# Kernel optimization log

Hardware: AMD Instinct MI355X
Metric: run time of the kernel (lower is better)

## Reference

```python
import jax, jax.numpy as jnp
import numpy as np

# Render constants matching GaussianRenderer(__init__): image size and top-K blend depth.
H, W, K = 128, 128, 10
N_G = 2048  # number of gaussians


def setup_inputs() -> dict:
    key = jax.random.key(0)
    k1, k2, k3, k4 = jax.random.split(key, 4)
    # Means in pixel coordinates so gaussians cover the image.
    gaussian_means = jax.random.uniform(k1, (N_G, 2), dtype=jnp.float32) * jnp.array([W, H], jnp.float32)
    # Rotation angle per gaussian in [0, 2pi).
    gaussian_rotations = jax.random.uniform(k2, (N_G,), dtype=jnp.float32) * (2.0 * np.pi)
    # log std-devs centered at log(3) => ~3px footprint.
    gaussian_log_scales = jax.random.normal(k3, (N_G, 2), dtype=jnp.float32) * 0.3 + np.log(3.0)
    gaussian_colors = jax.random.uniform(k4, (N_G, 3), dtype=jnp.float32)
    return {
        "gaussian_means": gaussian_means,
        "gaussian_rotations": gaussian_rotations,
        "gaussian_log_scales": gaussian_log_scales,
        "gaussian_colors": gaussian_colors,
    }


def reference(gaussian_means, gaussian_rotations, gaussian_log_scales, gaussian_colors):
    """2D Gaussian splatting: per-pixel top-K gaussians by opacity, alpha-composited.

    Covariance per gaussian: Sigma = R(theta) diag(exp(2*log_scales)) R(theta)^T.
    alpha_i(p) = exp(-0.5 * d^T Sigma^{-1} d), d = p - mean_i.
    Per pixel, the K gaussians with largest alpha are blended front-to-back:
        out = sum_i color_i * alpha_i * prod_{j<i} (1 - alpha_j).
    (The torch module's tile binning + max_G_per_tile is a GPU performance
    optimization; the dense evaluation here computes the same per-pixel math.)
    """
    cos_t = jnp.cos(gaussian_rotations)  # [N]
    sin_t = jnp.sin(gaussian_rotations)
    inv_var = jnp.exp(-2.0 * gaussian_log_scales)  # [N,2] = 1/sigma^2 per axis
    ivx, ivy = inv_var[:, 0], inv_var[:, 1]
    # Sigma^{-1} = R diag(1/sx^2, 1/sy^2) R^T  (symmetric 2x2: [[a, b], [b, c]])
    a = cos_t * cos_t * ivx + sin_t * sin_t * ivy  # [N]
    c = sin_t * sin_t * ivx + cos_t * cos_t * ivy
    b = cos_t * sin_t * (ivx - ivy)

    xs = jnp.arange(W, dtype=jnp.float32) + 0.5
    ys = jnp.arange(H, dtype=jnp.float32) + 0.5
    px, py = jnp.meshgrid(xs, ys)  # [H,W] each
    dx = px.reshape(-1, 1) - gaussian_means[:, 0]  # [P, N], P = H*W
    dy = py.reshape(-1, 1) - gaussian_means[:, 1]
    q = a * dx * dx + 2.0 * b * dx * dy + c * dy * dy  # Mahalanobis distance^2 [P,N]
    alpha = jnp.exp(-0.5 * q)  # [P,N] in (0,1]

    top_alpha, top_idx = jax.lax.top_k(alpha, K)  # [P,K], descending alpha
    # Front-to-back transmittance: T_0 = 1, T_i = prod_{j<i} (1 - alpha_j)
    trans = jnp.cumprod(1.0 - top_alpha, axis=1)
    trans = jnp.concatenate([jnp.ones_like(trans[:, :1]), trans[:, :-1]], axis=1)
    weight = top_alpha * trans  # [P,K]
    top_colors = gaussian_colors[top_idx]  # [P,K,3]
    image = jnp.einsum("pk,pkc->pc", weight, top_colors).reshape(H, W, 3)
    return image
```

## Files before the change

kernel.cpp:

```cpp
#include <hip/hip_runtime.h>

#define HH 128
#define WW 128
#define NPX (HH * WW)
#define KK 10
#define PXB 16
#define LCAP 352
#define JMAX 22
#define KEYC 6
#define SCAP (16 * KEYC)
#define SPAD (SCAP + 1)
#define ALPHA_MIN 5e-4f
#define RADIUS_K 3.8990f

typedef unsigned long long u64;
typedef unsigned int u32;

__global__ __launch_bounds__(256) void precompute_kernel(
    const float* __restrict__ means, const float* __restrict__ rots,
    const float* __restrict__ lscales, int nG,
    float4* __restrict__ bbox4, float4* __restrict__ prm4) {
  int g = blockIdx.x * blockDim.x + threadIdx.x;
  if (g >= nG) return;
  const float2* m2 = (const float2*)means;
  const float2* l2 = (const float2*)lscales;
  float2 mg = m2[g];
  float2 lg = l2[g];
  float smx = __expf(fmaxf(lg.x, lg.y));
  float r = fmaf(RADIUS_K * 1.01f, smx, 0.05f);
  float th = rots[g];
  float s = __sinf(th), c = __cosf(th);
  float ivx = __expf(-2.0f * lg.x);
  float ivy = __expf(-2.0f * lg.y);
  bbox4[g] = make_float4(mg.x, mg.y, r * r, 0.0f);
  prm4[g] = make_float4(c * c * ivx + s * s * ivy,
                        2.0f * (c * s * (ivx - ivy)),
                        s * s * ivx + c * c * ivy, mg.x);
}

template <int NGC, bool PRE>
__global__ __launch_bounds__(256) void splat_kernel(
    const float* __restrict__ means, const float* __restrict__ rots,
    const float* __restrict__ lscales, const float* __restrict__ cols,
    const float4* __restrict__ bbox4, const float4* __restrict__ prm4,
    int nG_rt, float* __restrict__ out) {
  const int nG = NGC > 0 ? NGC : nG_rt;
  __shared__ float4 sA[LCAP];
  __shared__ float  sMy[LCAP];
  __shared__ int    glist[LCAP];
  __shared__ float2 sbuf[PXB][SPAD];
  __shared__ float2 wbuf[PXB][KK];
  __shared__ int    lcnt;

  int t = threadIdx.x;
  int lane = t & 63;
  int pl  = t >> 4;
  int tsl = t & 15;
  int tile = blockIdx.x;
  int x0 = (tile & 31) << 2, y0 = (tile >> 5) << 2;
  int x = x0 | (pl & 3), y = y0 | (pl >> 2);
  float px = (float)x + 0.5f, py = (float)y + 0.5f;

  if (t == 0) lcnt = 0;
  __syncthreads();

  float rx0 = (float)x0 + 0.5f, rx1 = (float)x0 + 3.5f;
  float ry0 = (float)y0 + 0.5f, ry1 = (float)y0 + 3.5f;
  if (PRE && NGC > 0) {
    constexpr int FR = ((NGC > 0 ? NGC : 1) + 255) / 256;
    float4 bb[FR];
#pragma unroll
    for (int j = 0; j < FR; ++j) {
      int g = t + (j << 8);
      bb[j] = (g < NGC) ? bbox4[g] : make_float4(-1e30f, -1e30f, 0.0f, 0.0f);
    }
#pragma unroll
    for (int j = 0; j < FR; ++j) {
      float4 b = bb[j];
      float cx = fminf(fmaxf(b.x, rx0), rx1) - b.x;
      float cy = fminf(fmaxf(b.y, ry0), ry1) - b.y;
      bool hit = (cx * cx + cy * cy <= b.z);
      u64 mask = __ballot(hit);
      if (mask) {
        int leader = __ffsll((unsigned long long)mask) - 1;
        int base;
        if (lane == leader) base = atomicAdd(&lcnt, __popcll(mask));
        base = __shfl(base, leader);
        if (hit) {
          int idx = base + __popcll(mask & ((1ull << lane) - 1ull));
          if (idx < LCAP) {
            int g = t + (j << 8);
            sA[idx] = prm4[g];
            sMy[idx] = b.y;
            glist[idx] = g;
          }
        }
      }
    }
  } else if (PRE) {
    for (int g = t; g < nG; g += 256) {
      float4 b = bbox4[g];
      float cx = fminf(fmaxf(b.x, rx0), rx1) - b.x;
      float cy = fminf(fmaxf(b.y, ry0), ry1) - b.y;
      bool hit = (cx * cx + cy * cy <= b.z);
      u64 mask = __ballot(hit);
      if (mask) {
        int leader = __ffsll((unsigned long long)mask) - 1;
        int base;
        if (lane == leader) base = atomicAdd(&lcnt, __popcll(mask));
        base = __shfl(base, leader);
        if (hit) {
          int idx = base + __popcll(mask & ((1ull << lane) - 1ull));
          if (idx < LCAP) {
            sA[idx] = prm4[g];
            sMy[idx] = b.y;
            glist[idx] = g;
          }
        }
      }
    }
  } else {
    const float2* m2 = (const float2*)means;
    const float2* l2 = (const float2*)lscales;
    for (int g = t; g < nG; g += 256) {
      float2 mg = m2[g];
      float2 lg = l2[g];
      float smx = __expf(fmaxf(lg.x, lg.y));
      float r = fmaf(RADIUS_K * 1.01f, smx, 0.05f);
      float cx = fminf(fmaxf(mg.x, rx0), rx1) - mg.x;
      float cy = fminf(fmaxf(mg.y, ry0), ry1) - mg.y;
      bool hit = (cx * cx + cy * cy <= r * r);
      u64 mask = __ballot(hit);
      if (mask) {
        int leader = __ffsll((unsigned long long)mask) - 1;
        int base;
        if (lane == leader) base = atomicAdd(&lcnt, __popcll(mask));
        base = __shfl(base, leader);
        if (hit) {
          int idx = base + __popcll(mask & ((1ull << lane) - 1ull));
          if (idx < LCAP) {
            float th = rots[g];
            float s = __sinf(th), c = __cosf(th);
            float ivx = __expf(-2.0f * lg.x);
            float ivy = __expf(-2.0f * lg.y);
            sA[idx] = make_float4(c * c * ivx + s * s * ivy,
                                  2.0f * (c * s * (ivx - ivy)),
                                  s * s * ivx + c * c * ivy, mg.x);
            sMy[idx] = mg.y;
            glist[idx] = g;
          }
        }
      }
    }
  }
  __syncthreads();
  int cnt = min(lcnt, LCAP);
  int jcnt = (cnt + 15) >> 4;

  float ra[JMAX];
  float mymax = 0.0f;
#pragma unroll
  for (int j = 0; j < JMAX; ++j) {
    float a = 0.0f;
    if (j < jcnt) {
      int i = tsl + (j << 4);
      if (i < cnt) {
        float4 q0 = sA[i];
        float dx = px - q0.w, dy = py - sMy[i];
        float q = fmaf(dx, fmaf(q0.y, dy, q0.x * dx), q0.z * dy * dy);
        a = __expf(-0.5f * q);
      }
    }
    ra[j] = a;
    mymax = fmaxf(mymax, a);
  }

  float v = mymax;
#pragma unroll
  for (int k = 2; k <= 16; k <<= 1) {
#pragma unroll
    for (int j = k >> 1; j >= 1; j >>= 1) {
      float o = __shfl_xor(v, j, 16);
      bool keepMax = (((tsl & k) == 0) == ((tsl & j) == 0));
      v = keepMax ? fmaxf(v, o) : fminf(v, o);
    }
  }
  float tau = fmaxf(__shfl(v, 9, 16), ALPHA_MIN);

  int cpx = 0;
  int grp = lane >> 4;
#pragma unroll
  for (int j = 0; j < JMAX; ++j) {
    if (j < jcnt) {
      bool s = ra[j] >= tau;
      u64 mask = __ballot(s);
      u32 sub = (u32)((mask >> (grp * 16)) & 0xFFFFull);
      if (s) {
        int idx = cpx + __popc(sub & ((1u << tsl) - 1u));
        if (idx < SCAP)
          sbuf[pl][idx] = make_float2(ra[j], __int_as_float(glist[tsl + (j << 4)]));
      }
      cpx += __popc(sub);
    }
  }
  int scp = min(cpx, SCAP);
  int nw = min(scp, KK);

#pragma unroll
  for (int c = 0; c < KEYC; ++c) {
    if ((c << 4) < scp) {
      int i = tsl + (c << 4);
      u64 kc = 0;
      if (i < scp) {
        float2 e = sbuf[pl][i];
        kc = ((u64)__float_as_uint(e.x) << 32) | (u32)(~(u32)__float_as_int(e.y));
      }
      int rk = 0;
      for (int s2 = 0; s2 < scp; ++s2) {
        float2 e2 = sbuf[pl][s2];
        u64 ks2 = ((u64)__float_as_uint(e2.x) << 32) |
                  (u32)(~(u32)__float_as_int(e2.y));
        rk += (kc < ks2) ? 1 : 0;
      }
      if (kc != 0 && rk < KK)
        wbuf[pl][rk] = make_float2(__uint_as_float((u32)(kc >> 32)),
                                   __int_as_float((int)(~(u32)kc)));
    }
  }

  float my_alpha = 0.0f;
  int my_id = 0;
  if (tsl < nw) {
    float2 e = wbuf[pl][tsl];
    my_alpha = e.x;
    my_id = __float_as_int(e.y);
  }

  float T = 1.0f - my_alpha;
#pragma unroll
  for (int d = 1; d < 16; d <<= 1) {
    float u = __shfl_up(T, d, 16);
    if (tsl >= d) T *= u;
  }
  float ex = __shfl_up(T, 1, 16);
  if (tsl == 0) ex = 1.0f;
  float w = my_alpha * ex;
  float cr = 0.0f, cg = 0.0f, cb = 0.0f;
  if (my_alpha > 0.0f) {
    cr = w * cols[3 * my_id + 0];
    cg = w * cols[3 * my_id + 1];
    cb = w * cols[3 * my_id + 2];
  }
#pragma unroll
  for (int d = 1; d < 16; d <<= 1) {
    cr += __shfl_xor(cr, d);
    cg += __shfl_xor(cg, d);
    cb += __shfl_xor(cb, d);
  }
  int p = y * WW + x;
  if (tsl < 3) out[3 * p + tsl] = (tsl == 0) ? cr : ((tsl == 1) ? cg : cb);
}

extern "C" void kernel_launch(void* const* d_in, const int* in_sizes, int n_in,
                              void* d_out, int out_size, void* d_ws, size_t ws_size,
                              hipStream_t stream) {
  const float* means   = (const float*)d_in[0];
  const float* rots    = (const float*)d_in[1];
  const float* lscales = (const float*)d_in[2];
  const float* cols    = (const float*)d_in[3];
  float* out = (float*)d_out;
  int nG = in_sizes[1];

  size_t need = (size_t)nG * sizeof(float4) * 2;
  bool pre = (d_ws != nullptr) && (ws_size >= need);
  float4* bbox4 = (float4*)d_ws;
  float4* prm4 = (float4*)((char*)d_ws + (size_t)nG * sizeof(float4));

  if (pre)
    precompute_kernel<<<(nG + 255) / 256, 256, 0, stream>>>(means, rots,
                                                            lscales, nG,
                                                            bbox4, prm4);

  if (nG == 2048) {
    if (pre)
      splat_kernel<2048, true><<<NPX / PXB, 256, 0, stream>>>(
          means, rots, lscales, cols, bbox4, prm4, nG, out);
    else
      splat_kernel<2048, false><<<NPX / PXB, 256, 0, stream>>>(
          means, rots, lscales, cols, nullptr, nullptr, nG, out);
  } else {
    if (pre)
      splat_kernel<0, true><<<NPX / PXB, 256, 0, stream>>>(
          means, rots, lscales, cols, bbox4, prm4, nG, out);
    else
      splat_kernel<0, false><<<NPX / PXB, 256, 0, stream>>>(
          means, rots, lscales, cols, nullptr, nullptr, nG, out);
  }
}
```

Measured before the change: 69.75 us.

## Drop precompute kernel; compute conic params in-block after culling

Measured after the change: 68.22 us. 1.02x faster.

```diff
diff --git a/kernel.cpp b/kernel.cpp
--- a/kernel.cpp
+++ b/kernel.cpp
@@ -16,33 +16,10 @@
 typedef unsigned long long u64;
 typedef unsigned int u32;
 
-__global__ __launch_bounds__(256) void precompute_kernel(
-    const float* __restrict__ means, const float* __restrict__ rots,
-    const float* __restrict__ lscales, int nG,
-    float4* __restrict__ bbox4, float4* __restrict__ prm4) {
-  int g = blockIdx.x * blockDim.x + threadIdx.x;
-  if (g >= nG) return;
-  const float2* m2 = (const float2*)means;
-  const float2* l2 = (const float2*)lscales;
-  float2 mg = m2[g];
-  float2 lg = l2[g];
-  float smx = __expf(fmaxf(lg.x, lg.y));
-  float r = fmaf(RADIUS_K * 1.01f, smx, 0.05f);
-  float th = rots[g];
-  float s = __sinf(th), c = __cosf(th);
-  float ivx = __expf(-2.0f * lg.x);
-  float ivy = __expf(-2.0f * lg.y);
-  bbox4[g] = make_float4(mg.x, mg.y, r * r, 0.0f);
-  prm4[g] = make_float4(c * c * ivx + s * s * ivy,
-                        2.0f * (c * s * (ivx - ivy)),
-                        s * s * ivx + c * c * ivy, mg.x);
-}
-
-template <int NGC, bool PRE>
+template <int NGC>
 __global__ __launch_bounds__(256) void splat_kernel(
     const float* __restrict__ means, const float* __restrict__ rots,
     const float* __restrict__ lscales, const float* __restrict__ cols,
-    const float4* __restrict__ bbox4, const float4* __restrict__ prm4,
     int nG_rt, float* __restrict__ out) {
   const int nG = NGC > 0 ? NGC : nG_rt;
   __shared__ float4 sA[LCAP];
@@ -64,71 +41,26 @@
   if (t == 0) lcnt = 0;
   __syncthreads();
 
+  const float2* m2 = (const float2*)means;
+  const float2* l2 = (const float2*)lscales;
   float rx0 = (float)x0 + 0.5f, rx1 = (float)x0 + 3.5f;
   float ry0 = (float)y0 + 0.5f, ry1 = (float)y0 + 3.5f;
-  if (PRE && NGC > 0) {
+  if (NGC > 0) {
     constexpr int FR = ((NGC > 0 ? NGC : 1) + 255) / 256;
-    float4 bb[FR];
+    float2 mg[FR], lg[FR];
 #pragma unroll
     for (int j = 0; j < FR; ++j) {
       int g = t + (j << 8);
-      bb[j] = (g < NGC) ? bbox4[g] : make_float4(-1e30f, -1e30f, 0.0f, 0.0f);
+      bool v = g < NGC;
+      mg[j] = v ? m2[g] : make_float2(-1e30f, -1e30f);
+      lg[j] = v ? l2[g] : make_float2(0.0f, 0.0f);
     }
 #pragma unroll
     for (int j = 0; j < FR; ++j) {
-      float4 b = bb[j];
-      float cx = fminf(fmaxf(b.x, rx0), rx1) - b.x;
-      float cy = fminf(fmaxf(b.y, ry0), ry1) - b.y;
-      bool hit = (cx * cx + cy * cy <= b.z);
-      u64 mask = __ballot(hit);
-      if (mask) {
-        int leader = __ffsll((unsigned long long)mask) - 1;
-        int base;
-        if (lane == leader) base = atomicAdd(&lcnt, __popcll(mask));
-        base = __shfl(base, leader);
-        if (hit) {
-          int idx = base + __popcll(mask & ((1ull << lane) - 1ull));
-          if (idx < LCAP) {
-            int g = t + (j << 8);
-            sA[idx] = prm4[g];
-            sMy[idx] = b.y;
-            glist[idx] = g;
-          }
-        }
-      }
-    }
-  } else if (PRE) {
-    for (int g = t; g < nG; g += 256) {
-      float4 b = bbox4[g];
-      float cx = fminf(fmaxf(b.x, rx0), rx1) - b.x;
-      float cy = fminf(fmaxf(b.y, ry0), ry1) - b.y;
-      bool hit = (cx * cx + cy * cy <= b.z);
-      u64 mask = __ballot(hit);
-      if (mask) {
-        int leader = __ffsll((unsigned long long)mask) - 1;
-        int base;
-        if (lane == leader) base = atomicAdd(&lcnt, __popcll(mask));
-        base = __shfl(base, leader);
-        if (hit) {
-          int idx = base + __popcll(mask & ((1ull << lane) - 1ull));
-          if (idx < LCAP) {
-            sA[idx] = prm4[g];
-            sMy[idx] = b.y;
-            glist[idx] = g;
-          }
-        }
-      }
-    }
-  } else {
-    const float2* m2 = (const float2*)means;
-    const float2* l2 = (const float2*)lscales;
-    for (int g = t; g < nG; g += 256) {
-      float2 mg = m2[g];
-      float2 lg = l2[g];
-      float smx = __expf(fmaxf(lg.x, lg.y));
+      float smx = __expf(fmaxf(lg[j].x, lg[j].y));
       float r = fmaf(RADIUS_K * 1.01f, smx, 0.05f);
-      float cx = fminf(fmaxf(mg.x, rx0), rx1) - mg.x;
-      float cy = fminf(fmaxf(mg.y, ry0), ry1) - mg.y;
+      float cx = fminf(fmaxf(mg[j].x, rx0), rx1) - mg[j].x;
+      float cy = fminf(fmaxf(mg[j].y, ry0), ry1) - mg[j].y;
       bool hit = (cx * cx + cy * cy <= r * r);
       u64 mask = __ballot(hit);
       if (mask) {
@@ -139,14 +71,31 @@
         if (hit) {
           int idx = base + __popcll(mask & ((1ull << lane) - 1ull));
           if (idx < LCAP) {
-            float th = rots[g];
-            float s = __sinf(th), c = __cosf(th);
-            float ivx = __expf(-2.0f * lg.x);
-            float ivy = __expf(-2.0f * lg.y);
-            sA[idx] = make_float4(c * c * ivx + s * s * ivy,
-                                  2.0f * (c * s * (ivx - ivy)),
-                                  s * s * ivx + c * c * ivy, mg.x);
-            sMy[idx] = mg.y;
+            sMy[idx] = mg[j].y;
+            glist[idx] = t + (j << 8);
+          }
+        }
+      }
+    }
+  } else {
+    for (int g = t; g < nG; g += 256) {
+      float2 mgj = m2[g];
+      float2 lgj = l2[g];
+      float smx = __expf(fmaxf(lgj.x, lgj.y));
+      float r = fmaf(RADIUS_K * 1.01f, smx, 0.05f);
+      float cx = fminf(fmaxf(mgj.x, rx0), rx1) - mgj.x;
+      float cy = fminf(fmaxf(mgj.y, ry0), ry1) - mgj.y;
+      bool hit = (cx * cx + cy * cy <= r * r);
+      u64 mask = __ballot(hit);
+      if (mask) {
+        int leader = __ffsll((unsigned long long)mask) - 1;
+        int base;
+        if (lane == leader) base = atomicAdd(&lcnt, __popcll(mask));
+        base = __shfl(base, leader);
+        if (hit) {
+          int idx = base + __popcll(mask & ((1ull << lane) - 1ull));
+          if (idx < LCAP) {
+            sMy[idx] = mgj.y;
             glist[idx] = g;
           }
         }
@@ -155,6 +104,20 @@
   }
   __syncthreads();
   int cnt = min(lcnt, LCAP);
+
+  for (int i = t; i < cnt; i += 256) {
+    int g = glist[i];
+    float2 mgi = m2[g];
+    float2 lgi = l2[g];
+    float th = rots[g];
+    float s = __sinf(th), c = __cosf(th);
+    float ivx = __expf(-2.0f * lgi.x);
+    float ivy = __expf(-2.0f * lgi.y);
+    sA[i] = make_float4(c * c * ivx + s * s * ivy,
+                        2.0f * (c * s * (ivx - ivy)),
+                        s * s * ivx + c * c * ivy, mgi.x);
+  }
+  __syncthreads();
   int jcnt = (cnt + 15) >> 4;
 
   float ra[JMAX];
@@ -271,29 +234,11 @@
   float* out = (float*)d_out;
   int nG = in_sizes[1];
 
-  size_t need = (size_t)nG * sizeof(float4) * 2;
-  bool pre = (d_ws != nullptr) && (ws_size >= need);
-  float4* bbox4 = (float4*)d_ws;
-  float4* prm4 = (float4*)((char*)d_ws + (size_t)nG * sizeof(float4));
-
-  if (pre)
-    precompute_kernel<<<(nG + 255) / 256, 256, 0, stream>>>(means, rots,
-                                                            lscales, nG,
-                                                            bbox4, prm4);
-
   if (nG == 2048) {
-    if (pre)
-      splat_kernel<2048, true><<<NPX / PXB, 256, 0, stream>>>(
-          means, rots, lscales, cols, bbox4, prm4, nG, out);
-    else
-      splat_kernel<2048, false><<<NPX / PXB, 256, 0, stream>>>(
-          means, rots, lscales, cols, nullptr, nullptr, nG, out);
+    splat_kernel<2048><<<NPX / PXB, 256, 0, stream>>>(means, rots, lscales,
+                                                      cols, nG, out);
   } else {
-    if (pre)
-      splat_kernel<0, true><<<NPX / PXB, 256, 0, stream>>>(
-          means, rots, lscales, cols, bbox4, prm4, nG, out);
-    else
-      splat_kernel<0, false><<<NPX / PXB, 256, 0, stream>>>(
-          means, rots, lscales, cols, nullptr, nullptr, nG, out);
+    splat_kernel<0><<<NPX / PXB, 256, 0, stream>>>(means, rots, lscales,
+                                                   cols, nG, out);
   }
 }
```
